# Performance work log

Hardware: AMD Instinct MI355X
Metric: run time of the kernel (lower is better)

## Reference

```python
import jax, jax.numpy as jnp
import numpy as np

B, S, H = 4, 2048, 1024
NH = 16
DH = H // NH  # 64


def setup_inputs() -> dict:
    key = jax.random.key(0)
    ks = jax.random.split(key, 11)
    s = 1.0 / np.sqrt(H)
    inp = {
        "key": jax.random.normal(ks[0], (B, S, H), jnp.float32),
        "value": jax.random.normal(ks[1], (B, S, H), jnp.float32),
        "query": jax.random.normal(ks[2], (B, S, H), jnp.float32),
        # linear_layers[0] -> applied to query, [1] -> key, [2] -> value
        "wq": jax.random.normal(ks[3], (H, H), jnp.float32) * s,
        "bq": jnp.zeros((H,), jnp.float32),
        "wk": jax.random.normal(ks[4], (H, H), jnp.float32) * s,
        "bk": jnp.zeros((H,), jnp.float32),
        "wv": jax.random.normal(ks[5], (H, H), jnp.float32) * s,
        "bv": jnp.zeros((H,), jnp.float32),
        "wo": jax.random.normal(ks[6], (H, H), jnp.float32) * s,
        "bo": jnp.zeros((H,), jnp.float32),
    }
    return inp


def reference(key, value, query, wq, bq, wk, bk, wv, bv, wo, bo):
    # QKV projections; split heads -> [B, NH, S, DH]
    def proj(x, w, b):
        y = jnp.einsum("bsh,hd->bsd", x, w) + b
        return y.reshape(B, S, NH, DH).transpose(0, 2, 1, 3)

    q = proj(query, wq, bq)
    k = proj(key, wk, bk)
    v = proj(value, wv, bv)

    scores = jnp.einsum("bnqd,bnkd->bnqk", q, k) / jnp.sqrt(jnp.float32(DH))
    probs = jax.nn.softmax(scores, axis=-1)  # dropout p=0 -> identity
    out = jnp.einsum("bnqk,bnkd->bnqd", probs, v)
    out = out.transpose(0, 2, 1, 3).reshape(B, S, H)
    return jnp.einsum("bsh,hd->bsd", out, wo) + bo
```

## Files before the change

### kernel.cpp

```cpp
#include <hip/hip_runtime.h>
#include <hip/hip_bf16.h>

constexpr int kB = 4, kS = 2048, kH = 1024, kNH = 16, kDH = 64;
constexpr int kM = kB * kS;

typedef short short8 __attribute__((ext_vector_type(8)));
typedef float f32x4 __attribute__((ext_vector_type(4)));

__device__ inline unsigned int pack2bf16(float lo, float hi) {
  __hip_bfloat162 h;
  h.x = __float2bfloat16(lo);
  h.y = __float2bfloat16(hi);
  unsigned int u;
  __builtin_memcpy(&u, &h, 4);
  return u;
}

__device__ inline void gload_lds16(const unsigned short* g, unsigned short* l) {
  auto* gp = (const __attribute__((address_space(1))) unsigned int*)(uintptr_t)g;
  auto* lp = (__attribute__((address_space(3))) unsigned int*)(unsigned int)(uintptr_t)l;
  __builtin_amdgcn_global_load_lds(gp, lp, 16, 0, 0);
}

__global__ __launch_bounds__(256) void f32_to_bf16_vec(
    const float* __restrict__ in, __hip_bfloat16* __restrict__ out) {
  const int i = blockIdx.x * 256 + threadIdx.x;
  const float4 v = ((const float4*)in)[i];
  union { __hip_bfloat16 h[4]; uint2 u; } p;
  p.h[0] = __float2bfloat16(v.x);
  p.h[1] = __float2bfloat16(v.y);
  p.h[2] = __float2bfloat16(v.z);
  p.h[3] = __float2bfloat16(v.w);
  ((uint2*)out)[i] = p.u;
}

__global__ __launch_bounds__(256) void transpose4_f32_to_bf16(
    const float* __restrict__ w0, const float* __restrict__ w1,
    const float* __restrict__ w2, const float* __restrict__ w3,
    __hip_bfloat16* __restrict__ o0, __hip_bfloat16* __restrict__ o1,
    __hip_bfloat16* __restrict__ o2, __hip_bfloat16* __restrict__ o3) {
  const int z = blockIdx.z;
  const float* in = z == 0 ? w0 : z == 1 ? w1 : z == 2 ? w2 : w3;
  __hip_bfloat16* out = z == 0 ? o0 : z == 1 ? o1 : z == 2 ? o2 : o3;
  constexpr int R = kH, C = kH;
  __shared__ float t[32][33];
  const int r0 = blockIdx.y * 32, c0 = blockIdx.x * 32;
  const int tx = threadIdx.x, ty = threadIdx.y;
#pragma unroll
  for (int i = 0; i < 32; i += 8)
    t[ty + i][tx] = in[(size_t)(r0 + ty + i) * C + c0 + tx];
  __syncthreads();
#pragma unroll
  for (int i = 0; i < 32; i += 8)
    out[(size_t)(c0 + ty + i) * R + r0 + tx] = __float2bfloat16(t[tx][ty + i]);
}

template <int MODE, typename OutT>
__global__ __launch_bounds__(256) void gemm_mfma(
    const unsigned short* __restrict__ A,
    const unsigned short* __restrict__ Bt,
    const float* __restrict__ bias, OutT* __restrict__ C,
    int M, int N, int K, float oscale) {
  __shared__ unsigned short sA[128 * 32];
  __shared__ unsigned short sB[128 * 32];
  const int tid = threadIdx.x;
  const int wave = tid >> 6, lane = tid & 63;
  const int n16 = lane & 15, quad = lane >> 4;
  const int m0 = blockIdx.y * 128, n0 = blockIdx.x * 128;
  const int rh = (wave >> 1) * 64, ch = (wave & 1) * 64;

  const int srow = 32 * wave + (lane >> 2);
  const int sk = (lane & 3) * 8;
  const unsigned short* gA = A + (size_t)(m0 + srow) * K + sk;
  const unsigned short* gB = Bt + (size_t)(n0 + srow) * K + sk;

  const f32x4 zero4 = {0.f, 0.f, 0.f, 0.f};
  f32x4 acc[4][4];
#pragma unroll
  for (int i = 0; i < 4; ++i)
#pragma unroll
    for (int j = 0; j < 4; ++j) acc[i][j] = zero4;

  for (int k0 = 0; k0 < K; k0 += 32) {
    __syncthreads();
#pragma unroll
    for (int j = 0; j < 2; ++j) {
      gload_lds16(gA + (size_t)(16 * j) * K + k0, sA + (32 * wave + 16 * j) * 32);
      gload_lds16(gB + (size_t)(16 * j) * K + k0, sB + (32 * wave + 16 * j) * 32);
    }
    __syncthreads();

    short8 af[4], bfr[4];
#pragma unroll
    for (int i = 0; i < 4; ++i)
      af[i] = *(const short8*)&sA[(rh + i * 16 + n16) * 32 + quad * 8];
#pragma unroll
    for (int i = 0; i < 4; ++i)
      bfr[i] = *(const short8*)&sB[(ch + i * 16 + n16) * 32 + quad * 8];
#pragma unroll
    for (int mi = 0; mi < 4; ++mi)
#pragma unroll
      for (int ni = 0; ni < 4; ++ni)
        acc[mi][ni] = __builtin_amdgcn_mfma_f32_16x16x32_bf16(
            af[mi], bfr[ni], acc[mi][ni], 0, 0, 0);
  }

#pragma unroll
  for (int ni = 0; ni < 4; ++ni) {
    const int n = n0 + ch + ni * 16 + n16;
    const float bv = bias[n];
#pragma unroll
    for (int mi = 0; mi < 4; ++mi) {
      if constexpr (MODE == 2) {
        const int m = m0 + rh + mi * 16 + quad * 4;
        const int bb = m >> 11, ss = m & 2047;
        const int hh = n >> 6, dd = n & 63;
        const size_t idx = ((size_t)(bb * kNH + hh) * kDH + dd) * kS + ss;
        uint2 w;
        w.x = pack2bf16((acc[mi][ni][0] + bv) * oscale,
                        (acc[mi][ni][1] + bv) * oscale);
        w.y = pack2bf16((acc[mi][ni][2] + bv) * oscale,
                        (acc[mi][ni][3] + bv) * oscale);
        *(uint2*)&C[idx] = w;
      } else {
#pragma unroll
        for (int r = 0; r < 4; ++r) {
          const int m = m0 + rh + mi * 16 + quad * 4 + r;
          const float v = (acc[mi][ni][r] + bv) * oscale;
          size_t idx;
          if constexpr (MODE == 1) {
            const int bb = m >> 11, ss = m & 2047;
            const int hh = n >> 6, dd = n & 63;
            idx = ((size_t)(bb * kNH + hh) * kS + ss) * kDH + dd;
          } else {
            idx = (size_t)m * N + n;
          }
          C[idx] = (OutT)v;
        }
      }
    }
  }
}

__global__ __launch_bounds__(256) void attn_mfma(
    const unsigned short* __restrict__ Q, const unsigned short* __restrict__ K,
    const unsigned short* __restrict__ V, __hip_bfloat16* __restrict__ ctx) {
  __shared__ unsigned short sK[64][72];
  __shared__ unsigned short sVT[64][72];
  __shared__ unsigned short sP[4][16][72];

  const int tid = threadIdx.x;
  const int wave = tid >> 6, lane = tid & 63;
  const int n16 = lane & 15, quad = lane >> 4;
  const int bh = blockIdx.y;
  const int q0 = blockIdx.x * 64;
  const unsigned short* Qb = Q + (size_t)bh * (kS * kDH);
  const unsigned short* Kb = K + (size_t)bh * (kS * kDH);
  const unsigned short* Vb = V + (size_t)bh * (kS * kDH);

  short8 qf[2];
  {
    const size_t qoff = (size_t)(q0 + wave * 16 + n16) * kDH + quad * 8;
    qf[0] = *(const short8*)(Qb + qoff);
    qf[1] = *(const short8*)(Qb + qoff + 32);
  }

  float l_part = 0.f;
  f32x4 oacc[4];
  const f32x4 zero4 = {0.f, 0.f, 0.f, 0.f};
#pragma unroll
  for (int d = 0; d < 4; ++d) oacc[d] = zero4;

  const int srow = tid >> 2, scol = (tid & 3) * 16;

  for (int k0 = 0; k0 < kS; k0 += 64) {
    const uint4 ka = *(const uint4*)(Kb + (size_t)(k0 + srow) * kDH + scol);
    const uint4 kb = *(const uint4*)(Kb + (size_t)(k0 + srow) * kDH + scol + 8);
    const uint4 va = *(const uint4*)(Vb + (size_t)srow * kS + k0 + scol);
    const uint4 vb = *(const uint4*)(Vb + (size_t)srow * kS + k0 + scol + 8);
    __syncthreads();
    *(uint4*)&sK[srow][scol] = ka;
    *(uint4*)&sK[srow][scol + 8] = kb;
    *(uint4*)&sVT[srow][scol] = va;
    *(uint4*)&sVT[srow][scol + 8] = vb;
    __syncthreads();

    f32x4 sacc[4] = {zero4, zero4, zero4, zero4};
    __builtin_amdgcn_s_setprio(1);
#pragma unroll
    for (int c = 0; c < 2; ++c) {
#pragma unroll
      for (int nb = 0; nb < 4; ++nb) {
        const short8 af = *(const short8*)&sK[nb * 16 + n16][c * 32 + quad * 8];
        sacc[nb] = __builtin_amdgcn_mfma_f32_16x16x32_bf16(af, qf[c], sacc[nb], 0, 0, 0);
      }
    }
    __builtin_amdgcn_s_setprio(0);

#pragma unroll
    for (int nb = 0; nb < 4; ++nb) {
      float p0 = __builtin_amdgcn_exp2f(sacc[nb][0]);
      float p1 = __builtin_amdgcn_exp2f(sacc[nb][1]);
      float p2 = __builtin_amdgcn_exp2f(sacc[nb][2]);
      float p3 = __builtin_amdgcn_exp2f(sacc[nb][3]);
      l_part += (p0 + p1) + (p2 + p3);
      uint2 w;
      w.x = pack2bf16(p0, p1);
      w.y = pack2bf16(p2, p3);
      *(uint2*)&sP[wave][n16][nb * 16 + quad * 4] = w;
    }
    asm volatile("s_waitcnt lgkmcnt(0)" ::: "memory");
    __builtin_amdgcn_sched_barrier(0);

    __builtin_amdgcn_s_setprio(1);
#pragma unroll
    for (int c = 0; c < 2; ++c) {
      const short8 pf = *(const short8*)&sP[wave][n16][c * 32 + quad * 8];
#pragma unroll
      for (int d = 0; d < 4; ++d) {
        const short8 vf = *(const short8*)&sVT[d * 16 + n16][c * 32 + quad * 8];
        oacc[d] = __builtin_amdgcn_mfma_f32_16x16x32_bf16(vf, pf, oacc[d], 0, 0, 0);
      }
    }
    __builtin_amdgcn_s_setprio(0);
  }

  float l = l_part;
  l += __shfl_xor(l, 16);
  l += __shfl_xor(l, 32);
  const float inv = 1.f / l;

  const int bb = bh >> 4, hh = bh & 15;
  const int qrow = q0 + wave * 16 + n16;
  __hip_bfloat16* dst = ctx + ((size_t)(bb * kS + qrow)) * kH + hh * kDH;
#pragma unroll
  for (int d = 0; d < 4; ++d) {
    uint2 w;
    w.x = pack2bf16(oacc[d][0] * inv, oacc[d][1] * inv);
    w.y = pack2bf16(oacc[d][2] * inv, oacc[d][3] * inv);
    *(uint2*)(dst + d * 16 + quad * 4) = w;
  }
}

extern "C" void kernel_launch(void* const* d_in, const int* in_sizes, int n_in,
                              void* d_out, int out_size, void* d_ws, size_t ws_size,
                              hipStream_t stream) {
  const float* key   = (const float*)d_in[0];
  const float* value = (const float*)d_in[1];
  const float* query = (const float*)d_in[2];
  const float* wq = (const float*)d_in[3];
  const float* bq = (const float*)d_in[4];
  const float* wk = (const float*)d_in[5];
  const float* bk = (const float*)d_in[6];
  const float* wv = (const float*)d_in[7];
  const float* bv = (const float*)d_in[8];
  const float* wo = (const float*)d_in[9];
  const float* bo = (const float*)d_in[10];
  float* out = (float*)d_out;

  const size_t SZ = (size_t)kB * kS * kH;
  unsigned short* p = (unsigned short*)d_ws;
  unsigned short* actb = p; p += SZ;
  unsigned short* Qh   = p; p += SZ;
  unsigned short* Kh   = p; p += SZ;
  unsigned short* Vh   = p; p += SZ;
  unsigned short* ctxh = p; p += SZ;
  unsigned short* wqt  = p; p += (size_t)kH * kH;
  unsigned short* wkt  = p; p += (size_t)kH * kH;
  unsigned short* wvt  = p; p += (size_t)kH * kH;
  unsigned short* wot  = p; p += (size_t)kH * kH;

  const dim3 tb(32, 8);
  const dim3 tg(kH / 32, kH / 32, 4);
  transpose4_f32_to_bf16<<<tg, tb, 0, stream>>>(
      wq, wk, wv, wo, (__hip_bfloat16*)wqt, (__hip_bfloat16*)wkt,
      (__hip_bfloat16*)wvt, (__hip_bfloat16*)wot);

  const int cvblocks = (int)(SZ / 4 / 256);
  dim3 gg(kH / 128, kM / 128);

  constexpr float kQScale = 0.125f * 1.4426950408889634f;
  f32_to_bf16_vec<<<cvblocks, 256, 0, stream>>>(query, (__hip_bfloat16*)actb);
  gemm_mfma<1, __hip_bfloat16><<<gg, 256, 0, stream>>>(
      actb, wqt, bq, (__hip_bfloat16*)Qh, kM, kH, kH, kQScale);
  f32_to_bf16_vec<<<cvblocks, 256, 0, stream>>>(key, (__hip_bfloat16*)actb);
  gemm_mfma<1, __hip_bfloat16><<<gg, 256, 0, stream>>>(
      actb, wkt, bk, (__hip_bfloat16*)Kh, kM, kH, kH, 1.0f);
  f32_to_bf16_vec<<<cvblocks, 256, 0, stream>>>(value, (__hip_bfloat16*)actb);
  gemm_mfma<2, __hip_bfloat16><<<gg, 256, 0, stream>>>(
      actb, wvt, bv, (__hip_bfloat16*)Vh, kM, kH, kH, 1.0f);

  dim3 ga(kS / 64, kB * kNH);
  attn_mfma<<<ga, 256, 0, stream>>>(Qh, Kh, Vh, (__hip_bfloat16*)ctxh);

  gemm_mfma<0, float><<<gg, 256, 0, stream>>>(ctxh, wot, bo, out, kM, kH, kH, 1.0f);
}
```

Measured before the change: 411.1 us.

## Double-buffer GEMM LDS tiles and prefetch K/V tiles in attention loop

The GEMM now uses two LDS buffers per operand and issues the global-to-LDS loads for the next K-slice before computing on the current one, so there is one barrier per iteration instead of two. The attention kernel prefetches the next K/V tile into registers before the QK and PV MFMAs and writes it to shared memory after them, hiding global load latency behind compute. This costs double LDS in the GEMM and extra registers in attention. The GEMM relies on the single trailing barrier to order the async LDS writes against the reads, and the last iteration issues a harmless wraparound load.

Result: no change. 407.6 us (-0.9%).

```diff
diff --git a/kernel.cpp b/kernel.cpp
--- a/kernel.cpp
+++ b/kernel.cpp
@@ -61,8 +61,8 @@
     const unsigned short* __restrict__ Bt,
     const float* __restrict__ bias, OutT* __restrict__ C,
     int M, int N, int K, float oscale) {
-  __shared__ unsigned short sA[128 * 32];
-  __shared__ unsigned short sB[128 * 32];
+  __shared__ unsigned short sA[2][128 * 32];
+  __shared__ unsigned short sB[2][128 * 32];
   const int tid = threadIdx.x;
   const int wave = tid >> 6, lane = tid & 63;
   const int n16 = lane & 15, quad = lane >> 4;
@@ -81,28 +81,40 @@
 #pragma unroll
     for (int j = 0; j < 4; ++j) acc[i][j] = zero4;
 
+#pragma unroll
+  for (int j = 0; j < 2; ++j) {
+    gload_lds16(gA + (size_t)(16 * j) * K, &sA[0][(32 * wave + 16 * j) * 32]);
+    gload_lds16(gB + (size_t)(16 * j) * K, &sB[0][(32 * wave + 16 * j) * 32]);
+  }
+  __syncthreads();
+
+  int cur = 0;
   for (int k0 = 0; k0 < K; k0 += 32) {
-    __syncthreads();
+    const int kn = (k0 + 32 < K) ? k0 + 32 : 0;
 #pragma unroll
     for (int j = 0; j < 2; ++j) {
-      gload_lds16(gA + (size_t)(16 * j) * K + k0, sA + (32 * wave + 16 * j) * 32);
-      gload_lds16(gB + (size_t)(16 * j) * K + k0, sB + (32 * wave + 16 * j) * 32);
-    }
-    __syncthreads();
+      gload_lds16(gA + (size_t)(16 * j) * K + kn,
+                  &sA[cur ^ 1][(32 * wave + 16 * j) * 32]);
+      gload_lds16(gB + (size_t)(16 * j) * K + kn,
+                  &sB[cur ^ 1][(32 * wave + 16 * j) * 32]);
+    }
 
     short8 af[4], bfr[4];
 #pragma unroll
     for (int i = 0; i < 4; ++i)
-      af[i] = *(const short8*)&sA[(rh + i * 16 + n16) * 32 + quad * 8];
+      af[i] = *(const short8*)&sA[cur][(rh + i * 16 + n16) * 32 + quad * 8];
 #pragma unroll
     for (int i = 0; i < 4; ++i)
-      bfr[i] = *(const short8*)&sB[(ch + i * 16 + n16) * 32 + quad * 8];
+      bfr[i] = *(const short8*)&sB[cur][(ch + i * 16 + n16) * 32 + quad * 8];
 #pragma unroll
     for (int mi = 0; mi < 4; ++mi)
 #pragma unroll
       for (int ni = 0; ni < 4; ++ni)
         acc[mi][ni] = __builtin_amdgcn_mfma_f32_16x16x32_bf16(
             af[mi], bfr[ni], acc[mi][ni], 0, 0, 0);
+
+    __syncthreads();
+    cur ^= 1;
   }
 
 #pragma unroll
@@ -173,17 +185,27 @@
 
   const int srow = tid >> 2, scol = (tid & 3) * 16;
 
-  for (int k0 = 0; k0 < kS; k0 += 64) {
-    const uint4 ka = *(const uint4*)(Kb + (size_t)(k0 + srow) * kDH + scol);
-    const uint4 kb = *(const uint4*)(Kb + (size_t)(k0 + srow) * kDH + scol + 8);
-    const uint4 va = *(const uint4*)(Vb + (size_t)srow * kS + k0 + scol);
-    const uint4 vb = *(const uint4*)(Vb + (size_t)srow * kS + k0 + scol + 8);
-    __syncthreads();
+  uint4 ka, kb, va, vb;
+  auto loadtile = [&](int kk) {
+    ka = *(const uint4*)(Kb + (size_t)(kk + srow) * kDH + scol);
+    kb = *(const uint4*)(Kb + (size_t)(kk + srow) * kDH + scol + 8);
+    va = *(const uint4*)(Vb + (size_t)srow * kS + kk + scol);
+    vb = *(const uint4*)(Vb + (size_t)srow * kS + kk + scol + 8);
+  };
+  auto writetile = [&]() {
     *(uint4*)&sK[srow][scol] = ka;
     *(uint4*)&sK[srow][scol + 8] = kb;
     *(uint4*)&sVT[srow][scol] = va;
     *(uint4*)&sVT[srow][scol + 8] = vb;
-    __syncthreads();
+  };
+
+  loadtile(0);
+  writetile();
+  __syncthreads();
+
+  for (int k0 = 0; k0 < kS; k0 += 64) {
+    const int kn = (k0 + 64 < kS) ? k0 + 64 : 0;
+    loadtile(kn);
 
     f32x4 sacc[4] = {zero4, zero4, zero4, zero4};
     __builtin_amdgcn_s_setprio(1);
@@ -223,6 +245,10 @@
       }
     }
     __builtin_amdgcn_s_setprio(0);
+
+    __syncthreads();
+    writetile();
+    __syncthreads();
   }
 
   float l = l_part;
```
